# Kernel optimization log

Measured on AMD Instinct MI355X. Metric: run time of the kernel, lower is better.

## Reference

```python
import jax, jax.numpy as jnp
import numpy as np

M, D, A, H = 16384, 256, 264, 8
HD = A // H  # 33
B = 512
THRESH = 0.1
DECAY = 0.95


def setup_inputs() -> dict:
    key = jax.random.key(0)
    ks = jax.random.split(key, 16)
    rn = lambda i, shape, scale=1.0: jax.random.normal(ks[i], shape, dtype=jnp.float32) * scale
    return {
        "features": rn(0, (B, D)),
        "gradients": rn(1, (B, D), 0.1),
        "mem_keys": rn(2, (M, D)),
        "mem_values": rn(3, (M, D)),
        "mem_ages": jax.random.uniform(ks[4], (M,), dtype=jnp.float32, minval=0.0, maxval=50.0),
        "mem_surprise": jax.random.uniform(ks[5], (M,), dtype=jnp.float32, minval=0.0, maxval=5.0),
        "Wk": rn(6, (D, D), 1.0 / np.sqrt(D)), "bk": jnp.zeros((D,), jnp.float32),
        "Wv": rn(7, (D, D), 1.0 / np.sqrt(D)), "bv": jnp.zeros((D,), jnp.float32),
        "Wp": rn(8, (D, A), 1.0 / np.sqrt(D)), "bp": jnp.zeros((A,), jnp.float32),
        "Win": rn(9, (A, 3 * A), 1.0 / np.sqrt(A)), "b_in": jnp.zeros((3 * A,), jnp.float32),
        "Wout": rn(10, (A, A), 1.0 / np.sqrt(A)), "bout": jnp.zeros((A,), jnp.float32),
        "Wo": rn(11, (A, D), 1.0 / np.sqrt(A)), "bo": jnp.zeros((D,), jnp.float32),
    }


def reference(features, gradients, mem_keys, mem_values, mem_ages, mem_surprise,
              Wk, bk, Wv, bv, Wp, bp, Win, b_in, Wout, bout, Wo, bo):
    # ---- compute_surprise: grad norm * min cdist to memory keys ----
    d2 = (jnp.sum(features * features, 1)[:, None]
          + jnp.sum(mem_keys * mem_keys, 1)[None, :]
          - 2.0 * features @ mem_keys.T)                      # [B, M]
    min_dist = jnp.sqrt(jnp.clip(jnp.min(d2, axis=1), 0.0))   # [B]
    surprise = jnp.linalg.norm(gradients, axis=-1) * min_dist  # [B]
    memorize = surprise > THRESH                               # [B] bool

    # ---- write_memory: sequential per-item eviction (argmin of decayed surprise) ----
    def step(carry, xs):
        mk, mv, ages, surp = carry
        feat, s_i, w = xs
        slot = jnp.argmin(surp * DECAY ** ages)
        mk = mk.at[slot].set(jnp.where(w, feat @ Wk + bk, mk[slot]))
        mv = mv.at[slot].set(jnp.where(w, feat @ Wv + bv, mv[slot]))
        ages = ages.at[slot].set(jnp.where(w, 0.0, ages[slot]))
        surp = surp.at[slot].set(jnp.where(w, s_i, surp[slot]))
        return (mk, mv, ages, surp), None

    (mem_keys, mem_values, mem_ages, mem_surprise), _ = jax.lax.scan(
        step, (mem_keys, mem_values, mem_ages, mem_surprise),
        (features, surprise, memorize))

    # ---- read_memory: project, 8-head cross attention (1 query vs M slots) ----
    q = features @ Wp + bp        # [B, A]
    kf = mem_keys @ Wp + bp       # [M, A]
    vf = mem_values @ Wp + bp     # [M, A]
    Wq_, Wk_, Wv_ = jnp.split(Win, 3, axis=1)
    bq_, bk_, bv_ = jnp.split(b_in, 3)
    qh = (q @ Wq_ + bq_).reshape(B, H, HD)
    kh = (kf @ Wk_ + bk_).reshape(M, H, HD)
    vh = (vf @ Wv_ + bv_).reshape(M, H, HD)
    scores = jnp.einsum('bhd,mhd->bhm', qh, kh) / np.float32(np.sqrt(HD))
    attn = jax.nn.softmax(scores, axis=-1)                    # [B, H, M]
    ctx = jnp.einsum('bhm,mhd->bhd', attn, vh).reshape(B, A)
    retrieved = (ctx @ Wout + bout) @ Wo + bo                 # [B, D]
    return retrieved
```

## Files before the change

kernel.cpp:

```cpp
#include <hip/hip_runtime.h>
#include <math.h>
#include <stdint.h>

typedef unsigned short ushort_t;
typedef float v4f __attribute__((ext_vector_type(4)));
typedef short v8s __attribute__((ext_vector_type(8)));

#define ATTN_MS 16

__device__ __forceinline__ unsigned fenc(float f){
  unsigned b = __float_as_uint(f);
  return (b & 0x80000000u) ? ~b : (b | 0x80000000u);
}
__device__ __forceinline__ float fdec(unsigned u){
  unsigned b = (u & 0x80000000u) ? (u ^ 0x80000000u) : ~u;
  return __uint_as_float(b);
}
__device__ __forceinline__ ushort_t bf16_rne(float x){
  unsigned u = __float_as_uint(x);
  unsigned r = u + 0x7FFFu + ((u >> 16) & 1u);
  return (ushort_t)(r >> 16);
}
__device__ __forceinline__ void split2(float x, ushort_t& h, ushort_t& l){
  unsigned u = __float_as_uint(x);
  unsigned r = u + 0x7FFFu + ((u >> 16) & 1u);
  h = (ushort_t)(r >> 16);
  float hf = __uint_as_float(r & 0xFFFF0000u);
  l = bf16_rne(x - hf);
}
__device__ __forceinline__ float bf2f(ushort_t x){ return __uint_as_float(((unsigned)x) << 16); }
union U8 { v8s v; ushort_t u[8]; };

__device__ __forceinline__ void gl2lds16(const void* g, void* l){
  __builtin_amdgcn_global_load_lds(
      (const __attribute__((address_space(1))) unsigned int*)(uintptr_t)g,
      (__attribute__((address_space(3))) unsigned int*)(unsigned int)(uintptr_t)l,
      16, 0, 0);
}

__global__ __launch_bounds__(256) void prep_all(
    const float* __restrict__ features, const float* __restrict__ gradients,
    const float* __restrict__ mem_keys, const float* __restrict__ mem_values,
    ushort_t* __restrict__ FH, ushort_t* __restrict__ FL,
    ushort_t* __restrict__ MKH, ushort_t* __restrict__ MKL,
    ushort_t* __restrict__ MVH, ushort_t* __restrict__ MVL,
    float* __restrict__ k2, float* __restrict__ f2, float* __restrict__ gn,
    unsigned* __restrict__ minD2, ushort_t* __restrict__ VtGH, ushort_t* __restrict__ VtGL){
  int y = blockIdx.y, bx = blockIdx.x, t = threadIdx.x;
  if (y == 3){
    if (bx >= 3840) return;
    const int PER4 = 8*15*16384/4;
    int idx = bx*256 + t;
    if (idx >= 2*PER4) return;
    ushort_t* base = (idx < PER4) ? VtGH : VtGL;
    int i = (idx < PER4) ? idx : idx - PER4;
    int s = i*4;
    int hh = s / (15*16384);
    int r2 = s - hh*(15*16384);
    int row = 33 + (r2 >> 14);
    int col = r2 & 16383;
    ushort4 z; z.x = 0; z.y = 0; z.z = 0; z.w = 0;
    *(ushort4*)(base + (size_t)(hh*48 + row)*16384 + col) = z;
    return;
  }
  int wid = t >> 6, lane = t & 63;
  int row = bx*4 + wid;
  if (y == 2 && bx >= 128) return;
  const float* src = (y == 0) ? mem_keys : (y == 1) ? mem_values : features;
  float4 v = *(const float4*)(src + (size_t)row*256 + lane*4);
  ushort_t h0,h1,h2,h3,l0,l1,l2,l3;
  split2(v.x,h0,l0); split2(v.y,h1,l1); split2(v.z,h2,l2); split2(v.w,h3,l3);
  uint2 hp = make_uint2((unsigned)h0 | ((unsigned)h1<<16), (unsigned)h2 | ((unsigned)h3<<16));
  uint2 lp = make_uint2((unsigned)l0 | ((unsigned)l1<<16), (unsigned)l2 | ((unsigned)l3<<16));
  ushort_t* H = (y == 0) ? MKH : (y == 1) ? MVH : FH;
  ushort_t* L = (y == 0) ? MKL : (y == 1) ? MVL : FL;
  *(uint2*)(H + (size_t)row*256 + lane*4) = hp;
  *(uint2*)(L + (size_t)row*256 + lane*4) = lp;
  if (y == 1) return;
  float s = v.x*v.x + v.y*v.y + v.z*v.z + v.w*v.w;
  if (y == 0){
    for (int off = 32; off > 0; off >>= 1) s += __shfl_down(s, off, 64);
    if (lane == 0) k2[row] = s;
  } else {
    float4 g = *(const float4*)(gradients + (size_t)row*256 + lane*4);
    float tg = g.x*g.x + g.y*g.y + g.z*g.z + g.w*g.w;
    for (int off = 32; off > 0; off >>= 1){ s += __shfl_down(s, off, 64); tg += __shfl_down(tg, off, 64); }
    if (lane == 0){ f2[row] = s; gn[row] = sqrtf(tg); minD2[row] = 0xFFFFFFFFu; }
  }
}

__global__ __launch_bounds__(256) void gemm_bias(const float* __restrict__ A, const float* __restrict__ W,
                                                 const float* __restrict__ bias, float* __restrict__ C,
                                                 const float* __restrict__ W2, const float* __restrict__ bias2,
                                                 float* __restrict__ C2,
                                                 int M, int K, int N, int ldw, int woff){
  if (blockIdx.z == 1){ W = W2; bias = bias2; C = C2; }
  __shared__ float As[32*68];
  __shared__ float Ws[32*68];
  int m0 = blockIdx.x*64, c0 = blockIdx.y*64;
  int t = threadIdx.x;
  int mq = (t & 15)*4, cq = (t >> 4)*4;
  float acc[16];
  #pragma unroll
  for (int i = 0; i < 16; ++i) acc[i] = 0.f;
  for (int k0 = 0; k0 < K; k0 += 32){
    #pragma unroll
    for (int i = 0; i < 2; ++i){
      int idx = t + 256*i;
      int row = idx >> 3, kk = (idx & 7)*4;
      int gm = m0 + row, gk = k0 + kk;
      float x=0.f, y=0.f, z=0.f, w=0.f;
      if (gm < M){
        const float* ap = A + (size_t)gm*K + gk;
        if (gk + 3 < K){ float4 v = *(const float4*)ap; x=v.x; y=v.y; z=v.z; w=v.w; }
        else {
          if (gk   < K) x = ap[0];
          if (gk+1 < K) y = ap[1];
          if (gk+2 < K) z = ap[2];
          if (gk+3 < K) w = ap[3];
        }
      }
      As[(kk+0)*68+row]=x; As[(kk+1)*68+row]=y; As[(kk+2)*68+row]=z; As[(kk+3)*68+row]=w;
    }
    #pragma unroll
    for (int i = 0; i < 2; ++i){
      int idx = t + 256*i;
      int kk = idx >> 4, cc = (idx & 15)*4;
      int gk = k0 + kk, gc = c0 + cc;
      float4 v = make_float4(0.f,0.f,0.f,0.f);
      if (gk < K){
        const float* wp = W + (size_t)gk*ldw + woff + gc;
        if (gc + 3 < N) v = *(const float4*)wp;
        else {
          if (gc   < N) v.x = wp[0];
          if (gc+1 < N) v.y = wp[1];
          if (gc+2 < N) v.z = wp[2];
          if (gc+3 < N) v.w = wp[3];
        }
      }
      *(float4*)(Ws + kk*68 + cc) = v;
    }
    __syncthreads();
    #pragma unroll
    for (int j = 0; j < 32; ++j){
      float4 a = *(const float4*)(As + j*68 + mq);
      float4 w = *(const float4*)(Ws + j*68 + cq);
      acc[ 0]+=a.x*w.x; acc[ 1]+=a.x*w.y; acc[ 2]+=a.x*w.z; acc[ 3]+=a.x*w.w;
      acc[ 4]+=a.y*w.x; acc[ 5]+=a.y*w.y; acc[ 6]+=a.y*w.z; acc[ 7]+=a.y*w.w;
      acc[ 8]+=a.z*w.x; acc[ 9]+=a.z*w.y; acc[10]+=a.z*w.z; acc[11]+=a.z*w.w;
      acc[12]+=a.w*w.x; acc[13]+=a.w*w.y; acc[14]+=a.w*w.z; acc[15]+=a.w*w.w;
    }
    __syncthreads();
  }
  #pragma unroll
  for (int i = 0; i < 4; ++i){
    int gm = m0 + mq + i;
    if (gm >= M) continue;
    #pragma unroll
    for (int j = 0; j < 4; ++j){
      int gc = c0 + cq + j;
      if (gc >= N) continue;
      C[(size_t)gm*N + gc] = acc[i*4+j] + (bias ? bias[gc] : 0.f);
    }
  }
}

__global__ __launch_bounds__(256) void wprep_gemm(
    const float* __restrict__ Wp, const float* __restrict__ Win,
    const float* __restrict__ Wout, const float* __restrict__ Wo,
    const float* __restrict__ bp, const float* __restrict__ b_in,
    const float* __restrict__ bout, const float* __restrict__ bo,
    ushort_t* __restrict__ WtkH, ushort_t* __restrict__ WtkL,
    ushort_t* __restrict__ WtvH, ushort_t* __restrict__ WtvL,
    ushort_t* __restrict__ WtqH, ushort_t* __restrict__ WtqL,
    float* __restrict__ Wpk, float* __restrict__ Wpv, float* __restrict__ Wco,
    float* __restrict__ bpq, float* __restrict__ bpk, float* __restrict__ bpv, float* __restrict__ bco){
  __shared__ float As[32*68];
  __shared__ float Ws[32*68];
  int z = blockIdx.z;
  int t = threadIdx.x;
  if (z == 4){
    int flat = (blockIdx.x*5 + blockIdx.y)*256 + t;
    if (flat < 264){
      float a = b_in[flat];
      for (int k = 0; k < 264; ++k) a += bp[k]*Win[(size_t)k*792 + flat];
      bpq[flat] = a;
    } else if (flat < 528){
      int c = flat - 264;
      float a = b_in[264 + c];
      for (int k = 0; k < 264; ++k) a += bp[k]*Win[(size_t)k*792 + 264 + c];
      bpk[c] = a;
    } else if (flat < 792){
      int c = flat - 528;
      float a = b_in[528 + c];
      for (int k = 0; k < 264; ++k) a += bp[k]*Win[(size_t)k*792 + 528 + c];
      bpv[c] = a;
    } else if (flat < 1048){
      int c = flat - 792;
      float a = bo[c];
      for (int k = 0; k < 264; ++k) a += bout[k]*Wo[(size_t)k*256 + c];
      bco[c] = a;
    }
    return;
  }
  const float* A = (z < 3) ? Wp : Wout;
  const float* W = (z < 3) ? Win : Wo;
  const int M = (z < 3) ? 256 : 264;
  const int K = 264;
  const int N = (z < 3) ? 264 : 256;
  const int ldw = (z < 3) ? 792 : 256;
  const int woff = (z == 0) ? 264 : (z == 1) ? 528 : 0;
  int m0 = blockIdx.x*64, c0 = blockIdx.y*64;
  int mq = (t & 15)*4, cq = (t >> 4)*4;
  float acc[16];
  #pragma unroll
  for (int i = 0; i < 16; ++i) acc[i] = 0.f;
  for (int k0 = 0; k0 < K; k0 += 32){
    #pragma unroll
    for (int i = 0; i < 2; ++i){
      int idx = t + 256*i;
      int row = idx >> 3, kk = (idx & 7)*4;
      int gm = m0 + row, gk = k0 + kk;
      float x=0.f, y=0.f, z2=0.f, w=0.f;
      if (gm < M){
        const float* ap = A + (size_t)gm*K + gk;
        if (gk + 3 < K){ float4 v = *(const float4*)ap; x=v.x; y=v.y; z2=v.z; w=v.w; }
        else {
          if (gk   < K) x = ap[0];
          if (gk+1 < K) y = ap[1];
          if (gk+2 < K) z2 = ap[2];
          if (gk+3 < K) w = ap[3];
        }
      }
      As[(kk+0)*68+row]=x; As[(kk+1)*68+row]=y; As[(kk+2)*68+row]=z2; As[(kk+3)*68+row]=w;
    }
    #pragma unroll
    for (int i = 0; i < 2; ++i){
      int idx = t + 256*i;
      int kk = idx >> 4, cc = (idx & 15)*4;
      int gk = k0 + kk, gc = c0 + cc;
      float4 v = make_float4(0.f,0.f,0.f,0.f);
      if (gk < K){
        const float* wp = W + (size_t)gk*ldw + woff + gc;
        if (gc + 3 < N) v = *(const float4*)wp;
        else {
          if (gc   < N) v.x = wp[0];
          if (gc+1 < N) v.y = wp[1];
          if (gc+2 < N) v.z = wp[2];
          if (gc+3 < N) v.w = wp[3];
        }
      }
      *(float4*)(Ws + kk*68 + cc) = v;
    }
    __syncthreads();
    #pragma unroll
    for (int j = 0; j < 32; ++j){
      float4 a = *(const float4*)(As + j*68 + mq);
      float4 w = *(const float4*)(Ws + j*68 + cq);
      acc[ 0]+=a.x*w.x; acc[ 1]+=a.x*w.y; acc[ 2]+=a.x*w.z; acc[ 3]+=a.x*w.w;
      acc[ 4]+=a.y*w.x; acc[ 5]+=a.y*w.y; acc[ 6]+=a.y*w.z; acc[ 7]+=a.y*w.w;
      acc[ 8]+=a.z*w.x; acc[ 9]+=a.z*w.y; acc[10]+=a.z*w.z; acc[11]+=a.z*w.w;
      acc[12]+=a.w*w.x; acc[13]+=a.w*w.y; acc[14]+=a.w*w.z; acc[15]+=a.w*w.w;
    }
    __syncthreads();
  }
  if (z < 3){
    ushort_t* WH = (z==0) ? WtkH : (z==1) ? WtvH : WtqH;
    ushort_t* WL = (z==0) ? WtkL : (z==1) ? WtvL : WtqL;
    float* Wf = (z==0) ? Wpk : (z==1) ? Wpv : nullptr;
    #pragma unroll
    for (int i = 0; i < 4; ++i){
      int gm = m0 + mq + i;
      if (gm >= 256) continue;
      #pragma unroll
      for (int j = 0; j < 4; ++j){
        int gc = c0 + cq + j;
        float r = acc[i*4+j];
        ushort_t hh, ll; split2(r, hh, ll);
        WH[(size_t)gc*256 + gm] = hh;
        WL[(size_t)gc*256 + gm] = ll;
        if (Wf && gc < 264) Wf[(size_t)gm*264 + gc] = r;
      }
    }
  } else {
    #pragma unroll
    for (int i = 0; i < 4; ++i){
      int gm = m0 + mq + i;
      if (gm >= 264) continue;
      #pragma unroll
      for (int j = 0; j < 4; ++j){
        int gc = c0 + cq + j;
        if (gc < 256) Wco[(size_t)gm*256 + gc] = acc[i*4+j];
      }
    }
  }
}

__global__ __launch_bounds__(256, 4) void big_mfma(
    const ushort_t* __restrict__ FH, const ushort_t* __restrict__ FL,
    const ushort_t* __restrict__ MKH, const ushort_t* __restrict__ MKL,
    const ushort_t* __restrict__ MVH, const ushort_t* __restrict__ MVL,
    const ushort_t* __restrict__ WtqH, const ushort_t* __restrict__ WtqL,
    const ushort_t* __restrict__ WtkH, const ushort_t* __restrict__ WtkL,
    const ushort_t* __restrict__ WtvH, const ushort_t* __restrict__ WtvL,
    const float* __restrict__ bpq, const float* __restrict__ bpk, const float* __restrict__ bpv,
    const float* __restrict__ k2,
    float* __restrict__ qh, ushort_t* __restrict__ khH, ushort_t* __restrict__ khL,
    ushort_t* __restrict__ VtGH, ushort_t* __restrict__ VtGL, unsigned* __restrict__ minD2){
  int z = blockIdx.z;
  int bx = blockIdx.x, by = blockIdx.y;
  if (z == 0 && bx >= 4) return;
  if (z != 3 && by >= 5) return;
  __shared__ ushort_t AsH[128*32];
  __shared__ ushort_t AsL[128*32];
  __shared__ ushort_t BsH[64*32];
  __shared__ ushort_t BsL[64*32];
  __shared__ unsigned sminU[64];
  const ushort_t* AH = (z == 0) ? FH : (z == 2) ? MVH : MKH;
  const ushort_t* AL = (z == 0) ? FL : (z == 2) ? MVL : MKL;
  const ushort_t* BH = (z == 0) ? WtqH : (z == 1) ? WtkH : (z == 2) ? WtvH : FH;
  const ushort_t* BL = (z == 0) ? WtqL : (z == 1) ? WtkL : WtvL;
  const float* bias = (z == 0) ? bpq : (z == 1) ? bpk : bpv;
  int t = threadIdx.x;
  int m0 = bx*128, n0 = by*64;
  int lane = t & 63, w = t >> 6;
  int wm = (w & 1)*64, wn = (w >> 1)*32;
  int l15 = lane & 15, q = lane >> 4;
  if (z == 3 && t < 64) sminU[t] = 0xFFFFFFFFu;
  v4f acc[4][2];
  #pragma unroll
  for (int i = 0; i < 4; ++i)
    #pragma unroll
    for (int j = 0; j < 2; ++j) acc[i][j] = (v4f){0.f,0.f,0.f,0.f};

  for (int k0 = 0; k0 < 256; k0 += 32){
    #pragma unroll
    for (int c = 0; c < 2; ++c){
      int u0 = (c*4 + w)*64;
      int u  = u0 + lane;
      int row = u >> 2, ch = u & 3;
      gl2lds16(AH + (size_t)(m0+row)*256 + k0 + ch*8, AsH + (size_t)u0*8);
      if (z < 3) gl2lds16(AL + (size_t)(m0+row)*256 + k0 + ch*8, AsL + (size_t)u0*8);
    }
    {
      int u = w*64 + lane;
      int row = u >> 2, ch = u & 3;
      gl2lds16(BH + (size_t)(n0+row)*256 + k0 + ch*8, BsH + (size_t)w*512);
      if (z < 3) gl2lds16(BL + (size_t)(n0+row)*256 + k0 + ch*8, BsL + (size_t)w*512);
    }
    __syncthreads();
    if (z < 3){
      v8s aH[4], aL[4], bH[2], bL[2];
      #pragma unroll
      for (int im = 0; im < 4; ++im){
        aH[im] = *(const v8s*)(AsH + (wm + im*16 + l15)*32 + q*8);
        aL[im] = *(const v8s*)(AsL + (wm + im*16 + l15)*32 + q*8);
      }
      #pragma unroll
      for (int jn = 0; jn < 2; ++jn){
        bH[jn] = *(const v8s*)(BsH + (wn + jn*16 + l15)*32 + q*8);
        bL[jn] = *(const v8s*)(BsL + (wn + jn*16 + l15)*32 + q*8);
      }
      #pragma unroll
      for (int im = 0; im < 4; ++im)
        #pragma unroll
        for (int jn = 0; jn < 2; ++jn){
          acc[im][jn] = __builtin_amdgcn_mfma_f32_16x16x32_bf16(aH[im], bH[jn], acc[im][jn], 0, 0, 0);
          acc[im][jn] = __builtin_amdgcn_mfma_f32_16x16x32_bf16(aH[im], bL[jn], acc[im][jn], 0, 0, 0);
          acc[im][jn] = __builtin_amdgcn_mfma_f32_16x16x32_bf16(aL[im], bH[jn], acc[im][jn], 0, 0, 0);
        }
    } else {
      v8s aH[4], bH[2];
      #pragma unroll
      for (int im = 0; im < 4; ++im) aH[im] = *(const v8s*)(AsH + (wm + im*16 + l15)*32 + q*8);
      #pragma unroll
      for (int jn = 0; jn < 2; ++jn) bH[jn] = *(const v8s*)(BsH + (wn + jn*16 + l15)*32 + q*8);
      #pragma unroll
      for (int im = 0; im < 4; ++im)
        #pragma unroll
        for (int jn = 0; jn < 2; ++jn)
          acc[im][jn] = __builtin_amdgcn_mfma_f32_16x16x32_bf16(aH[im], bH[jn], acc[im][jn], 0, 0, 0);
    }
    __syncthreads();
  }

  if (z == 3){
    float kk[4][4];
    #pragma unroll
    for (int im = 0; im < 4; ++im)
      #pragma unroll
      for (int r = 0; r < 4; ++r) kk[im][r] = k2[m0 + wm + im*16 + q*4 + r];
    #pragma unroll
    for (int jn = 0; jn < 2; ++jn){
      float mv = INFINITY;
      #pragma unroll
      for (int im = 0; im < 4; ++im)
        #pragma unroll
        for (int r = 0; r < 4; ++r)
          mv = fminf(mv, kk[im][r] - 2.f*acc[im][jn][r]);
      mv = fminf(mv, __shfl_xor(mv, 16, 64));
      mv = fminf(mv, __shfl_xor(mv, 32, 64));
      if (q == 0) atomicMin(&sminU[wn + jn*16 + l15], fenc(mv));
    }
    __syncthreads();
    if (t < 64) atomicMin(&minD2[n0 + t], sminU[t]);
    return;
  }
  #pragma unroll
  for (int im = 0; im < 4; ++im){
    #pragma unroll
    for (int jn = 0; jn < 2; ++jn){
      int n = n0 + wn + jn*16 + l15;
      if (n >= 264) continue;
      float bv = bias[n];
      int mb = m0 + wm + im*16 + q*4;
      if (z == 0){
        #pragma unroll
        for (int r = 0; r < 4; ++r) qh[(size_t)(mb+r)*264 + n] = acc[im][jn][r] + bv;
      } else if (z == 1){
        int hh = n/33, dd = n - hh*33;
        int col = hh*40 + dd;
        #pragma unroll
        for (int r = 0; r < 4; ++r){
          ushort_t sh, sl; split2(acc[im][jn][r] + bv, sh, sl);
          khH[(size_t)(mb+r)*320 + col] = sh;
          khL[(size_t)(mb+r)*320 + col] = sl;
        }
      } else {
        int hh = n/33, dd = n - hh*33;
        size_t rowb = (size_t)(hh*48 + dd)*16384 + mb;
        ushort4 hv, lv;
        split2(acc[im][jn][0] + bv, hv.x, lv.x);
        split2(acc[im][jn][1] + bv, hv.y, lv.y);
        split2(acc[im][jn][2] + bv, hv.z, lv.z);
        split2(acc[im][jn][3] + bv, hv.w, lv.w);
        *(ushort4*)(VtGH + rowb) = hv;
        *(ushort4*)(VtGL + rowb) = lv;
      }
    }
  }
}

#define SCAN_CAP 1024
__global__ __launch_bounds__(1024) void scan_kernel(
    const float* __restrict__ mem_surprise, const float* __restrict__ mem_ages,
    const unsigned* __restrict__ minD2, const float* __restrict__ f2, const float* __restrict__ gn,
    float* __restrict__ parr, int* __restrict__ slotForB, int* __restrict__ lastB){
  __shared__ unsigned hist[2048];
  __shared__ float candV[SCAN_CAP];
  __shared__ int   candI[SCAN_CAP];
  __shared__ float tv[1024];
  __shared__ int   ti[1024];
  __shared__ float ssur[512];
  __shared__ int   smemz[512];
  __shared__ int   wtot[16];
  __shared__ int   sh_misc[8];
  int t = threadIdx.x;

  int mem = 0;
  if (t < 512){
    float d2 = fdec(minD2[t]) + f2[t];
    float s = gn[t]*sqrtf(fmaxf(d2, 0.f));
    ssur[t] = s;
    mem = (s > 0.1f) ? 1 : 0;
    smemz[t] = mem;
  }
  const float LN095 = -0.05129329438755058f;
  #pragma unroll
  for (int j = 0; j < 16; ++j){
    int m = t*16 + j;
    float p = mem_surprise[m] * __expf(mem_ages[m] * LN095);
    parr[m] = p;
    lastB[m] = -1;
  }
  hist[t] = 0u; hist[t + 1024] = 0u;
  if (t < 8) sh_misc[t] = (t == 3) ? 0x7F800000 : 0;
  __syncthreads();
  #pragma unroll
  for (int j = 0; j < 16; ++j){
    int m = t*16 + j;
    unsigned key = __float_as_uint(parr[m]) >> 20;
    if (key > 2047u) key = 2047u;
    atomicAdd(&hist[key], 1u);
  }
  __syncthreads();
  if (t < 512){ ti[t] = (int)(hist[4*t] + hist[4*t+1] + hist[4*t+2] + hist[4*t+3]); }
  __syncthreads();
  if (t < 32){ int s = 0; for (int i = 0; i < 16; ++i) s += ti[16*t + i]; ti[512 + t] = s; }
  __syncthreads();
  if (t == 0){
    int cum = 0, i2 = 0;
    for (; i2 < 32; ++i2){ if (cum + ti[512+i2] >= 512) break; cum += ti[512+i2]; }
    int i1 = i2*16;
    for (;; ++i1){ if (cum + ti[i1] >= 512) break; cum += ti[i1]; }
    int bin = i1*4;
    for (;; ++bin){ if (cum + (int)hist[bin] >= 512) break; cum += (int)hist[bin]; }
    sh_misc[1] = bin;
  }
  __syncthreads();
  int threshKey = sh_misc[1];
  #pragma unroll
  for (int j = 0; j < 16; ++j){
    int m = t*16 + j;
    unsigned key = __float_as_uint(parr[m]) >> 20;
    if (key > 2047u) key = 2047u;
    if ((int)key <= threshKey){
      int pos = atomicAdd(&sh_misc[0], 1);
      if (pos < SCAN_CAP){ candV[pos] = parr[m]; candI[pos] = m; }
    }
  }
  __syncthreads();
  int cnt = sh_misc[0];
  if (t >= cnt && t < SCAN_CAP){ candV[t] = INFINITY; candI[t] = 0x7FFFFFFF; }
  __syncthreads();
  for (int ksz = 2; ksz <= SCAN_CAP; ksz <<= 1){
    for (int jj = ksz >> 1; jj > 0; jj >>= 1){
      int ixj = t ^ jj;
      if (ixj > t){
        float v1 = candV[t], v2 = candV[ixj];
        int i1 = candI[t], i2 = candI[ixj];
        bool lt21 = (v2 < v1) || (v2 == v1 && i2 < i1);
        bool lt12 = (v1 < v2) || (v1 == v2 && i1 < i2);
        bool up = ((t & ksz) == 0);
        bool sw = up ? lt21 : lt12;
        if (sw){ candV[t] = v2; candI[t] = i2; candV[ixj] = v1; candI[ixj] = i1; }
      }
      __syncthreads();
    }
  }
  int lp = 0;
  if (t < 512){
    unsigned long long mask = __ballot(mem != 0);
    int lane = t & 63;
    lp = __popcll(mask & ((1ull << lane) - 1ull));
    if (lane == 0) wtot[t >> 6] = __popcll(mask);
  }
  if (t < 512 && mem) atomicMin(&sh_misc[3], __float_as_int(ssur[t]));
  __syncthreads();
  if (t == 0){
    int ksum = 0;
    for (int wv = 0; wv < 8; ++wv) ksum += wtot[wv];
    sh_misc[4] = ksum;
    bool okf = (cnt <= SCAN_CAP) && (ksum <= cnt);
    if (okf && ksum > 0){
      float minw = __int_as_float(sh_misc[3]);
      okf = (minw > candV[ksum - 1]);
    }
    sh_misc[2] = okf ? 1 : 0;
  }
  __syncthreads();
  if (sh_misc[2] == 1){
    if (t < 512){
      int wv = t >> 6, base = 0;
      for (int i = 0; i < wv; ++i) base += wtot[i];
      int slot = -1;
      if (mem){ slot = candI[base + lp]; atomicMax(&lastB[slot], t); }
      slotForB[t] = slot;
    }
  } else {
    for (int b = 0; b < 512; ++b){
      float bv = parr[t*16]; int bi = t*16;
      #pragma unroll
      for (int j = 1; j < 16; ++j){
        float v = parr[t*16 + j];
        if (v < bv){ bv = v; bi = t*16 + j; }
      }
      tv[t] = bv; ti[t] = bi;
      __syncthreads();
      for (int s = 512; s > 0; s >>= 1){
        if (t < s){
          float v2 = tv[t+s]; int i2 = ti[t+s];
          if (v2 < tv[t] || (v2 == tv[t] && i2 < ti[t])){ tv[t] = v2; ti[t] = i2; }
        }
        __syncthreads();
      }
      int slot = ti[0];
      int memb = smemz[b];
      if (t == 0) slotForB[b] = memb ? slot : -1;
      if (memb && t == (slot >> 4)) parr[slot] = ssur[b];
      __syncthreads();
    }
    if (t < 512){ int s = slotForB[t]; if (s >= 0) atomicMax(&lastB[s], t); }
  }
}

__global__ __launch_bounds__(64) void fixup_rows(const int* __restrict__ slotForB, const int* __restrict__ lastB,
                                                 const float* __restrict__ newK, const float* __restrict__ newV,
                                                 const float* __restrict__ Wpk, const float* __restrict__ Wpv,
                                                 const float* __restrict__ bpk, const float* __restrict__ bpv,
                                                 ushort_t* __restrict__ khH, ushort_t* __restrict__ khL,
                                                 ushort_t* __restrict__ VtH, ushort_t* __restrict__ VtL){
  int b = blockIdx.x;
  int slot = slotForB[b];
  if (slot < 0) return;
  if (lastB[slot] != b) return;
  __shared__ float kr[256], vr[256];
  int t = threadIdx.x;
  *(float4*)(kr + t*4) = *(const float4*)(newK + (size_t)b*256 + t*4);
  *(float4*)(vr + t*4) = *(const float4*)(newV + (size_t)b*256 + t*4);
  __syncthreads();
  for (int c = t; c < 264; c += 64){
    float aK = bpk[c], aV = bpv[c];
    for (int k = 0; k < 256; ++k){
      aK += kr[k]*Wpk[(size_t)k*264 + c];
      aV += vr[k]*Wpv[(size_t)k*264 + c];
    }
    int hh = c/33, dd = c - hh*33;
    ushort_t sh, sl;
    split2(aK, sh, sl);
    khH[(size_t)slot*320 + hh*40 + dd] = sh;
    khL[(size_t)slot*320 + hh*40 + dd] = sl;
    split2(aV, sh, sl);
    VtH[(size_t)(hh*48 + dd)*16384 + slot] = sh;
    VtL[(size_t)(hh*48 + dd)*16384 + slot] = sl;
  }
}

__global__ __launch_bounds__(256, 4) void attn_mfma(
    const float* __restrict__ qh, const ushort_t* __restrict__ khH, const ushort_t* __restrict__ khL,
    const ushort_t* __restrict__ VtGH, const ushort_t* __restrict__ VtGL,
    float* __restrict__ pm, float* __restrict__ pl, float* __restrict__ pctx){
  const int h = blockIdx.x, bt = blockIdx.y, ms = blockIdx.z;
  const int b0 = bt*64, mbase = ms*(16384/ATTN_MS);
  const int t = threadIdx.x, lane = t & 63, w = t >> 6;
  const int l15 = lane & 15, q = lane >> 4;
  __shared__ ushort_t KH[64*32], KL[64*32];
  __shared__ ushort_t VsH[48*64], VsL[48*64];
  __shared__ ushort_t PH[4*16*72], PL[4*16*72];
  __shared__ float k32f[64];
  const float scale = 0.17407765595569785f;

  const int bq = b0 + 16*w + l15;
  U8 qHU, qLU;
  {
    const float* qp = qh + (size_t)bq*264 + h*33 + q*8;
    #pragma unroll
    for (int j = 0; j < 8; ++j) split2(qp[j]*scale, qHU.u[j], qLU.u[j]);
  }
  const v8s bQH = qHU.v, bQL = qLU.v;
  const float q32v = qh[(size_t)bq*264 + h*33 + 32]*scale;
  float rMv = -INFINITY, rLv = 0.f;
  v4f cacc[3];
  #pragma unroll
  for (int i = 0; i < 3; ++i) cacc[i] = (v4f){0.f,0.f,0.f,0.f};
  ushort_t* PHw = PH + w*16*72;
  ushort_t* PLw = PL + w*16*72;

  for (int mt = 0; mt < 16384/ATTN_MS/64; ++mt){
    const int m0 = mbase + mt*64;
    __syncthreads();
    {
      int u = w*64 + lane;
      int row = u >> 2, ch = u & 3;
      gl2lds16(khH + (size_t)(m0+row)*320 + h*40 + ch*8, KH + (size_t)w*512);
      gl2lds16(khL + (size_t)(m0+row)*320 + h*40 + ch*8, KL + (size_t)w*512);
    }
    if (t < 64)
      k32f[t] = bf2f(khH[(size_t)(m0+t)*320 + h*40 + 32]) + bf2f(khL[(size_t)(m0+t)*320 + h*40 + 32]);
    #pragma unroll
    for (int c = 0; c < 2; ++c){
      if (c == 0 || w < 2){
        int u0 = c*256 + w*64;
        int u = u0 + lane;
        int dd = u >> 3, chl = u & 7;
        int gch = chl ^ (dd & 7);
        size_t gi = (size_t)(h*48 + dd)*16384 + m0 + gch*8;
        gl2lds16(VtGH + gi, VsH + (size_t)u0*8);
        gl2lds16(VtGL + gi, VsL + (size_t)u0*8);
      }
    }
    __syncthreads();
    v4f s4[4];
    #pragma unroll
    for (int im = 0; im < 4; ++im){
      v8s aH = *(const v8s*)(KH + (im*16 + l15)*32 + q*8);
      v8s aL = *(const v8s*)(KL + (im*16 + l15)*32 + q*8);
      v4f sv = (v4f){0.f,0.f,0.f,0.f};
      sv = __builtin_amdgcn_mfma_f32_16x16x32_bf16(aH, bQH, sv, 0, 0, 0);
      sv = __builtin_amdgcn_mfma_f32_16x16x32_bf16(aH, bQL, sv, 0, 0, 0);
      sv = __builtin_amdgcn_mfma_f32_16x16x32_bf16(aL, bQH, sv, 0, 0, 0);
      s4[im] = sv;
    }
    #pragma unroll
    for (int im = 0; im < 4; ++im)
      #pragma unroll
      for (int r = 0; r < 4; ++r) s4[im][r] += k32f[im*16 + q*4 + r]*q32v;
    float mx = -INFINITY;
    #pragma unroll
    for (int im = 0; im < 4; ++im)
      #pragma unroll
      for (int r = 0; r < 4; ++r) mx = fmaxf(mx, s4[im][r]);
    mx = fmaxf(mx, __shfl_xor(mx, 16, 64));
    mx = fmaxf(mx, __shfl_xor(mx, 32, 64));
    float nm = fmaxf(rMv, mx);
    float alf = __expf(rMv - nm);
    rMv = nm;
    float sm = 0.f;
    #pragma unroll
    for (int im = 0; im < 4; ++im){
      v4f p;
      #pragma unroll
      for (int r = 0; r < 4; ++r){ p[r] = __expf(s4[im][r] - nm); sm += p[r]; }
      ushort4 hv, lv;
      split2(p[0], hv.x, lv.x); split2(p[1], hv.y, lv.y);
      split2(p[2], hv.z, lv.z); split2(p[3], hv.w, lv.w);
      *(ushort4*)(PHw + l15*72 + im*16 + q*4) = hv;
      *(ushort4*)(PLw + l15*72 + im*16 + q*4) = lv;
    }
    sm += __shfl_xor(sm, 16, 64);
    sm += __shfl_xor(sm, 32, 64);
    rLv = rLv*alf + sm;
    #pragma unroll
    for (int r = 0; r < 4; ++r){
      float ar = __shfl(alf, q*4 + r, 64);
      cacc[0][r] *= ar; cacc[1][r] *= ar; cacc[2][r] *= ar;
    }
    #pragma unroll
    for (int ks = 0; ks < 2; ++ks){
      v8s paH = *(const v8s*)(PHw + l15*72 + ks*32 + q*8);
      v8s paL = *(const v8s*)(PLw + l15*72 + ks*32 + q*8);
      #pragma unroll
      for (int tile = 0; tile < 3; ++tile){
        int vrow = tile*16 + l15;
        int mch = (ks*4 + q) ^ (l15 & 7);
        v8s vbH = *(const v8s*)(VsH + vrow*64 + mch*8);
        v8s vbL = *(const v8s*)(VsL + vrow*64 + mch*8);
        cacc[tile] = __builtin_amdgcn_mfma_f32_16x16x32_bf16(paH, vbH, cacc[tile], 0, 0, 0);
        cacc[tile] = __builtin_amdgcn_mfma_f32_16x16x32_bf16(paH, vbL, cacc[tile], 0, 0, 0);
        cacc[tile] = __builtin_amdgcn_mfma_f32_16x16x32_bf16(paL, vbH, cacc[tile], 0, 0, 0);
      }
    }
  }
  int g = (h*8 + bt)*ATTN_MS + ms;
  if (q == 0){
    pm[(size_t)g*64 + 16*w + l15] = rMv;
    pl[(size_t)g*64 + 16*w + l15] = rLv;
  }
  #pragma unroll
  for (int tile = 0; tile < 3; ++tile){
    int d = tile*16 + l15;
    if (d < 33){
      #pragma unroll
      for (int r = 0; r < 4; ++r)
        pctx[((size_t)g*64 + 16*w + q*4 + r)*33 + d] = cacc[tile][r];
    }
  }
}

__global__ __launch_bounds__(256) void combine_kernel(const float* __restrict__ pm, const float* __restrict__ pl,
                                                      const float* __restrict__ pctx, float* __restrict__ ctxf){
  int idx = blockIdx.x*256 + threadIdx.x;
  if (idx >= 512*264) return;
  int b = idx / 264, c = idx - b*264;
  int h = c / 33, d = c - h*33;
  int bt = b >> 6, bl = b & 63;
  int g0 = (h*8 + bt)*ATTN_MS;
  float gm = -INFINITY;
  for (int ms = 0; ms < ATTN_MS; ++ms) gm = fmaxf(gm, pm[(g0+ms)*64 + bl]);
  float L = 0.f, cv = 0.f;
  for (int ms = 0; ms < ATTN_MS; ++ms){
    int gg = (g0+ms)*64 + bl;
    float w = __expf(pm[gg] - gm);
    L += pl[gg]*w;
    cv += pctx[(size_t)gg*33 + d]*w;
  }
  ctxf[idx] = cv / L;
}

extern "C" void kernel_launch(void* const* d_in, const int* in_sizes, int n_in,
                              void* d_out, int out_size, void* d_ws, size_t ws_size,
                              hipStream_t stream){
  (void)in_sizes; (void)n_in; (void)out_size; (void)ws_size;
  const float* features     = (const float*)d_in[0];
  const float* gradients    = (const float*)d_in[1];
  const float* mem_keys     = (const float*)d_in[2];
  const float* mem_values   = (const float*)d_in[3];
  const float* mem_ages     = (const float*)d_in[4];
  const float* mem_surprise = (const float*)d_in[5];
  const float* Wk   = (const float*)d_in[6];
  const float* bk   = (const float*)d_in[7];
  const float* Wv   = (const float*)d_in[8];
  const float* bv   = (const float*)d_in[9];
  const float* Wp   = (const float*)d_in[10];
  const float* bp   = (const float*)d_in[11];
  const float* Win  = (const float*)d_in[12];
  const float* b_in = (const float*)d_in[13];
  const float* Wout = (const float*)d_in[14];
  const float* bout = (const float*)d_in[15];
  const float* Wo   = (const float*)d_in[16];
  const float* bo   = (const float*)d_in[17];
  float* out = (float*)d_out;

  float* w = (float*)d_ws;
  size_t off = 0;
  auto alloc = [&](size_t n)->float*{ float* p = w + off; off += (n + 63) & ~(size_t)63; return p; };
  float*    k2       = alloc(16384);
  unsigned* minD2    = (unsigned*)alloc(512);
  float*    f2       = alloc(512);
  float*    gn       = alloc(512);
  int*      slotForB = (int*)alloc(512);
  int*      lastB    = (int*)alloc(16384);
  float*    parr     = alloc(16384);
  float*    newK     = alloc((size_t)512*256);
  float*    newV     = alloc((size_t)512*256);
  float*    qh       = alloc((size_t)512*264);
  ushort_t* khH      = (ushort_t*)alloc((size_t)16384*320/2);
  ushort_t* khL      = (ushort_t*)alloc((size_t)16384*320/2);
  ushort_t* VtGH     = (ushort_t*)alloc((size_t)8*48*16384/2);
  ushort_t* VtGL     = (ushort_t*)alloc((size_t)8*48*16384/2);
  float*    MKbase   = alloc((size_t)16384*256/2*2);
  ushort_t* MKH      = (ushort_t*)MKbase;
  ushort_t* MKL      = (ushort_t*)(MKbase + (size_t)16384*256/2);
  float*    MVbase   = alloc((size_t)16384*256/2*2);
  ushort_t* MVH      = (ushort_t*)MVbase;
  ushort_t* MVL      = (ushort_t*)(MVbase + (size_t)16384*256/2);
  ushort_t* FH       = (ushort_t*)alloc((size_t)512*256/2);
  ushort_t* FL       = (ushort_t*)alloc((size_t)512*256/2);
  float*    Wpk      = alloc((size_t)256*264);
  float*    Wpv      = alloc((size_t)256*264);
  float*    Wco      = alloc((size_t)264*256);
  ushort_t* WtkH     = (ushort_t*)alloc((size_t)320*256/2);
  ushort_t* WtkL     = (ushort_t*)alloc((size_t)320*256/2);
  ushort_t* WtvH     = (ushort_t*)alloc((size_t)320*256/2);
  ushort_t* WtvL     = (ushort_t*)alloc((size_t)320*256/2);
  ushort_t* WtqH     = (ushort_t*)alloc((size_t)320*256/2);
  ushort_t* WtqL     = (ushort_t*)alloc((size_t)320*256/2);
  float*    bpq      = alloc(264);
  float*    bpk      = alloc(264);
  float*    bpv      = alloc(264);
  float*    bco      = alloc(256);
  float*    pm       = MKbase;
  float*    pl       = MKbase + (size_t)ATTN_MS*64*64;
  float*    ctxf     = pl + (size_t)ATTN_MS*64*64;
  float*    pctx     = MVbase;

  prep_all<<<dim3(4096,4), 256, 0, stream>>>(features, gradients, mem_keys, mem_values,
      FH, FL, MKH, MKL, MVH, MVL, k2, f2, gn, minD2, VtGH, VtGL);

  wprep_gemm<<<dim3(5,5,5), 256, 0, stream>>>(Wp, Win, Wout, Wo, bp, b_in, bout, bo,
      WtkH, WtkL, WtvH, WtvL, WtqH, WtqL, Wpk, Wpv, Wco, bpq, bpk, bpv, bco);

  gemm_bias<<<dim3(8,4,2), 256, 0, stream>>>(features, Wk, bk, newK, Wv, bv, newV, 512, 256, 256, 256, 0);

  big_mfma<<<dim3(128,8,4), 256, 0, stream>>>(FH, FL, MKH, MKL, MVH, MVL,
      WtqH, WtqL, WtkH, WtkL, WtvH, WtvL, bpq, bpk, bpv, k2,
      qh, khH, khL, VtGH, VtGL, minD2);

  scan_kernel<<<1, 1024, 0, stream>>>(mem_surprise, mem_ages, minD2, f2, gn, parr, slotForB, lastB);
  fixup_rows<<<512, 64, 0, stream>>>(slotForB, lastB, newK, newV, Wpk, Wpv, bpk, bpv, khH, khL, VtGH, VtGL);

  attn_mfma<<<dim3(8,8,ATTN_MS), 256, 0, stream>>>(qh, khH, khL, VtGH, VtGL, pm, pl, pctx);
  combine_kernel<<<528, 256, 0, stream>>>(pm, pl, pctx, ctxf);
  gemm_bias<<<dim3(8,4,1), 256, 0, stream>>>(ctxf, Wco, bco, out, Wco, bco, out, 512, 264, 256, 256, 0);
}
```

Measured before the change: 398.8 us.

## Fold Wk/Wv into projection weights, precompute replacement rows, drop V padding zeroing

Precomputes the combined weights Wk·Wpk and Wv·Wpv (plus biases) in a new wprep2 kernel. big_mfma then gets two extra z-slices that compute the projected replacement key and value rows for all 512 features with MFMA. fixup_rows becomes a plain copy instead of a serial 256-long dot product per column. It also removes the big zero-fill of VtG padding rows in prep_all, zeroing those rows once in LDS inside attn_mfma instead. The k32 scalar column is stored as fp32 in a separate buffer and loaded asynchronously, where before it was reconstructed from bf16 halves. The extra work is a few small launches and blocks, and replacement rows are now rounded through a folded weight product, which changes the rounding order slightly.

```diff
diff --git a/kernel.cpp b/kernel.cpp
--- a/kernel.cpp
+++ b/kernel.cpp
@@ -28,7 +28,6 @@
   float hf = __uint_as_float(r & 0xFFFF0000u);
   l = bf16_rne(x - hf);
 }
-__device__ __forceinline__ float bf2f(ushort_t x){ return __uint_as_float(((unsigned)x) << 16); }
 union U8 { v8s v; ushort_t u[8]; };
 
 __device__ __forceinline__ void gl2lds16(const void* g, void* l){
@@ -45,24 +44,8 @@
     ushort_t* __restrict__ MKH, ushort_t* __restrict__ MKL,
     ushort_t* __restrict__ MVH, ushort_t* __restrict__ MVL,
     float* __restrict__ k2, float* __restrict__ f2, float* __restrict__ gn,
-    unsigned* __restrict__ minD2, ushort_t* __restrict__ VtGH, ushort_t* __restrict__ VtGL){
+    unsigned* __restrict__ minD2){
   int y = blockIdx.y, bx = blockIdx.x, t = threadIdx.x;
-  if (y == 3){
-    if (bx >= 3840) return;
-    const int PER4 = 8*15*16384/4;
-    int idx = bx*256 + t;
-    if (idx >= 2*PER4) return;
-    ushort_t* base = (idx < PER4) ? VtGH : VtGL;
-    int i = (idx < PER4) ? idx : idx - PER4;
-    int s = i*4;
-    int hh = s / (15*16384);
-    int r2 = s - hh*(15*16384);
-    int row = 33 + (r2 >> 14);
-    int col = r2 & 16383;
-    ushort4 z; z.x = 0; z.y = 0; z.z = 0; z.w = 0;
-    *(ushort4*)(base + (size_t)(hh*48 + row)*16384 + col) = z;
-    return;
-  }
   int wid = t >> 6, lane = t & 63;
   int row = bx*4 + wid;
   if (y == 2 && bx >= 128) return;
@@ -91,10 +74,7 @@
 
 __global__ __launch_bounds__(256) void gemm_bias(const float* __restrict__ A, const float* __restrict__ W,
                                                  const float* __restrict__ bias, float* __restrict__ C,
-                                                 const float* __restrict__ W2, const float* __restrict__ bias2,
-                                                 float* __restrict__ C2,
                                                  int M, int K, int N, int ldw, int woff){
-  if (blockIdx.z == 1){ W = W2; bias = bias2; C = C2; }
   __shared__ float As[32*68];
   __shared__ float Ws[32*68];
   int m0 = blockIdx.x*64, c0 = blockIdx.y*64;
@@ -296,6 +276,91 @@
   }
 }
 
+__global__ __launch_bounds__(256) void wprep2(
+    const float* __restrict__ Wk, const float* __restrict__ Wv,
+    const float* __restrict__ Wpk, const float* __restrict__ Wpv,
+    const float* __restrict__ bk, const float* __restrict__ bv,
+    const float* __restrict__ bpk, const float* __restrict__ bpv,
+    ushort_t* __restrict__ WtfkH, ushort_t* __restrict__ WtfkL,
+    ushort_t* __restrict__ WtfvH, ushort_t* __restrict__ WtfvL,
+    float* __restrict__ bfk, float* __restrict__ bfv){
+  __shared__ float As[32*68];
+  __shared__ float Ws[32*68];
+  int z = blockIdx.z;
+  int t = threadIdx.x;
+  if (z == 2){
+    int flat = (blockIdx.x*5 + blockIdx.y)*256 + t;
+    if (flat < 264){
+      float a = bpk[flat];
+      for (int k = 0; k < 256; ++k) a += bk[k]*Wpk[(size_t)k*264 + flat];
+      bfk[flat] = a;
+    } else if (flat < 528){
+      int c = flat - 264;
+      float a = bpv[c];
+      for (int k = 0; k < 256; ++k) a += bv[k]*Wpv[(size_t)k*264 + c];
+      bfv[c] = a;
+    }
+    return;
+  }
+  if (blockIdx.x >= 4) return;
+  const float* A = z ? Wv : Wk;
+  const float* W = z ? Wpv : Wpk;
+  int m0 = blockIdx.x*64, c0 = blockIdx.y*64;
+  int mq = (t & 15)*4, cq = (t >> 4)*4;
+  float acc[16];
+  #pragma unroll
+  for (int i = 0; i < 16; ++i) acc[i] = 0.f;
+  for (int k0 = 0; k0 < 256; k0 += 32){
+    #pragma unroll
+    for (int i = 0; i < 2; ++i){
+      int idx = t + 256*i;
+      int row = idx >> 3, kk = (idx & 7)*4;
+      float4 v = *(const float4*)(A + (size_t)(m0+row)*256 + k0 + kk);
+      As[(kk+0)*68+row]=v.x; As[(kk+1)*68+row]=v.y; As[(kk+2)*68+row]=v.z; As[(kk+3)*68+row]=v.w;
+    }
+    #pragma unroll
+    for (int i = 0; i < 2; ++i){
+      int idx = t + 256*i;
+      int kk = idx >> 4, cc = (idx & 15)*4;
+      int gk = k0 + kk, gc = c0 + cc;
+      float4 v = make_float4(0.f,0.f,0.f,0.f);
+      const float* wp = W + (size_t)gk*264 + gc;
+      if (gc + 3 < 264) v = *(const float4*)wp;
+      else {
+        if (gc   < 264) v.x = wp[0];
+        if (gc+1 < 264) v.y = wp[1];
+        if (gc+2 < 264) v.z = wp[2];
+        if (gc+3 < 264) v.w = wp[3];
+      }
+      *(float4*)(Ws + kk*68 + cc) = v;
+    }
+    __syncthreads();
+    #pragma unroll
+    for (int j = 0; j < 32; ++j){
+      float4 a = *(const float4*)(As + j*68 + mq);
+      float4 w = *(const float4*)(Ws + j*68 + cq);
+      acc[ 0]+=a.x*w.x; acc[ 1]+=a.x*w.y; acc[ 2]+=a.x*w.z; acc[ 3]+=a.x*w.w;
+      acc[ 4]+=a.y*w.x; acc[ 5]+=a.y*w.y; acc[ 6]+=a.y*w.z; acc[ 7]+=a.y*w.w;
+      acc[ 8]+=a.z*w.x; acc[ 9]+=a.z*w.y; acc[10]+=a.z*w.z; acc[11]+=a.z*w.w;
+      acc[12]+=a.w*w.x; acc[13]+=a.w*w.y; acc[14]+=a.w*w.z; acc[15]+=a.w*w.w;
+    }
+    __syncthreads();
+  }
+  ushort_t* WH = z ? WtfvH : WtfkH;
+  ushort_t* WL = z ? WtfvL : WtfkL;
+  #pragma unroll
+  for (int i = 0; i < 4; ++i){
+    int gm = m0 + mq + i;
+    #pragma unroll
+    for (int j = 0; j < 4; ++j){
+      int gc = c0 + cq + j;
+      ushort_t hh, ll; split2(acc[i*4+j], hh, ll);
+      WH[(size_t)gc*256 + gm] = hh;
+      WL[(size_t)gc*256 + gm] = ll;
+    }
+  }
+}
+
 __global__ __launch_bounds__(256, 4) void big_mfma(
     const ushort_t* __restrict__ FH, const ushort_t* __restrict__ FL,
     const ushort_t* __restrict__ MKH, const ushort_t* __restrict__ MKL,
@@ -303,24 +368,29 @@
     const ushort_t* __restrict__ WtqH, const ushort_t* __restrict__ WtqL,
     const ushort_t* __restrict__ WtkH, const ushort_t* __restrict__ WtkL,
     const ushort_t* __restrict__ WtvH, const ushort_t* __restrict__ WtvL,
+    const ushort_t* __restrict__ WtfkH, const ushort_t* __restrict__ WtfkL,
+    const ushort_t* __restrict__ WtfvH, const ushort_t* __restrict__ WtfvL,
     const float* __restrict__ bpq, const float* __restrict__ bpk, const float* __restrict__ bpv,
+    const float* __restrict__ bfk, const float* __restrict__ bfv,
     const float* __restrict__ k2,
-    float* __restrict__ qh, ushort_t* __restrict__ khH, ushort_t* __restrict__ khL,
+    float* __restrict__ qh, float* __restrict__ khB, float* __restrict__ VtB,
+    ushort_t* __restrict__ khH, ushort_t* __restrict__ khL, float* __restrict__ k32g,
     ushort_t* __restrict__ VtGH, ushort_t* __restrict__ VtGL, unsigned* __restrict__ minD2){
   int z = blockIdx.z;
   int bx = blockIdx.x, by = blockIdx.y;
-  if (z == 0 && bx >= 4) return;
+  if ((z == 0 || z >= 4) && bx >= 4) return;
   if (z != 3 && by >= 5) return;
   __shared__ ushort_t AsH[128*32];
   __shared__ ushort_t AsL[128*32];
   __shared__ ushort_t BsH[64*32];
   __shared__ ushort_t BsL[64*32];
   __shared__ unsigned sminU[64];
-  const ushort_t* AH = (z == 0) ? FH : (z == 2) ? MVH : MKH;
-  const ushort_t* AL = (z == 0) ? FL : (z == 2) ? MVL : MKL;
-  const ushort_t* BH = (z == 0) ? WtqH : (z == 1) ? WtkH : (z == 2) ? WtvH : FH;
-  const ushort_t* BL = (z == 0) ? WtqL : (z == 1) ? WtkL : WtvL;
-  const float* bias = (z == 0) ? bpq : (z == 1) ? bpk : bpv;
+  const ushort_t* AH = (z == 2) ? MVH : (z == 1 || z == 3) ? MKH : FH;
+  const ushort_t* AL = (z == 2) ? MVL : (z == 1 || z == 3) ? MKL : FL;
+  const ushort_t* BH = (z==0) ? WtqH : (z==1) ? WtkH : (z==2) ? WtvH : (z==3) ? FH : (z==4) ? WtfkH : WtfvH;
+  const ushort_t* BL = (z==0) ? WtqL : (z==1) ? WtkL : (z==2) ? WtvL : (z==4) ? WtfkL : WtfvL;
+  const float* bias = (z==0) ? bpq : (z==1) ? bpk : (z==2) ? bpv : (z==4) ? bfk : bfv;
+  float* Cf = (z==0) ? qh : (z==4) ? khB : VtB;
   int t = threadIdx.x;
   int m0 = bx*128, n0 = by*64;
   int lane = t & 63, w = t >> 6;
@@ -340,16 +410,16 @@
       int u  = u0 + lane;
       int row = u >> 2, ch = u & 3;
       gl2lds16(AH + (size_t)(m0+row)*256 + k0 + ch*8, AsH + (size_t)u0*8);
-      if (z < 3) gl2lds16(AL + (size_t)(m0+row)*256 + k0 + ch*8, AsL + (size_t)u0*8);
+      if (z != 3) gl2lds16(AL + (size_t)(m0+row)*256 + k0 + ch*8, AsL + (size_t)u0*8);
     }
     {
       int u = w*64 + lane;
       int row = u >> 2, ch = u & 3;
       gl2lds16(BH + (size_t)(n0+row)*256 + k0 + ch*8, BsH + (size_t)w*512);
-      if (z < 3) gl2lds16(BL + (size_t)(n0+row)*256 + k0 + ch*8, BsL + (size_t)w*512);
-    }
-    __syncthreads();
-    if (z < 3){
+      if (z != 3) gl2lds16(BL + (size_t)(n0+row)*256 + k0 + ch*8, BsL + (size_t)w*512);
+    }
+    __syncthreads();
+    if (z != 3){
       v8s aH[4], aL[4], bH[2], bL[2];
       #pragma unroll
       for (int im = 0; im < 4; ++im){
@@ -414,19 +484,18 @@
       if (n >= 264) continue;
       float bv = bias[n];
       int mb = m0 + wm + im*16 + q*4;
-      if (z == 0){
-        #pragma unroll
-        for (int r = 0; r < 4; ++r) qh[(size_t)(mb+r)*264 + n] = acc[im][jn][r] + bv;
-      } else if (z == 1){
+      if (z == 1){
         int hh = n/33, dd = n - hh*33;
         int col = hh*40 + dd;
         #pragma unroll
         for (int r = 0; r < 4; ++r){
-          ushort_t sh, sl; split2(acc[im][jn][r] + bv, sh, sl);
+          float val = acc[im][jn][r] + bv;
+          ushort_t sh, sl; split2(val, sh, sl);
           khH[(size_t)(mb+r)*320 + col] = sh;
           khL[(size_t)(mb+r)*320 + col] = sl;
+          if (dd == 32) k32g[(size_t)hh*16384 + mb + r] = val;
         }
-      } else {
+      } else if (z == 2){
         int hh = n/33, dd = n - hh*33;
         size_t rowb = (size_t)(hh*48 + dd)*16384 + mb;
         ushort4 hv, lv;
@@ -436,6 +505,9 @@
         split2(acc[im][jn][3] + bv, hv.w, lv.w);
         *(ushort4*)(VtGH + rowb) = hv;
         *(ushort4*)(VtGL + rowb) = lv;
+      } else {
+        #pragma unroll
+        for (int r = 0; r < 4; ++r) Cf[(size_t)(mb+r)*264 + n] = acc[im][jn][r] + bv;
       }
     }
   }
@@ -585,32 +657,25 @@
 }
 
 __global__ __launch_bounds__(64) void fixup_rows(const int* __restrict__ slotForB, const int* __restrict__ lastB,
-                                                 const float* __restrict__ newK, const float* __restrict__ newV,
-                                                 const float* __restrict__ Wpk, const float* __restrict__ Wpv,
-                                                 const float* __restrict__ bpk, const float* __restrict__ bpv,
+                                                 const float* __restrict__ khB, const float* __restrict__ VtB,
                                                  ushort_t* __restrict__ khH, ushort_t* __restrict__ khL,
-                                                 ushort_t* __restrict__ VtH, ushort_t* __restrict__ VtL){
+                                                 ushort_t* __restrict__ VtH, ushort_t* __restrict__ VtL,
+                                                 float* __restrict__ k32g){
   int b = blockIdx.x;
   int slot = slotForB[b];
   if (slot < 0) return;
   if (lastB[slot] != b) return;
-  __shared__ float kr[256], vr[256];
   int t = threadIdx.x;
-  *(float4*)(kr + t*4) = *(const float4*)(newK + (size_t)b*256 + t*4);
-  *(float4*)(vr + t*4) = *(const float4*)(newV + (size_t)b*256 + t*4);
-  __syncthreads();
   for (int c = t; c < 264; c += 64){
-    float aK = bpk[c], aV = bpv[c];
-    for (int k = 0; k < 256; ++k){
-      aK += kr[k]*Wpk[(size_t)k*264 + c];
-      aV += vr[k]*Wpv[(size_t)k*264 + c];
-    }
     int hh = c/33, dd = c - hh*33;
+    float kv = khB[(size_t)b*264 + c];
     ushort_t sh, sl;
-    split2(aK, sh, sl);
+    split2(kv, sh, sl);
     khH[(size_t)slot*320 + hh*40 + dd] = sh;
     khL[(size_t)slot*320 + hh*40 + dd] = sl;
-    split2(aV, sh, sl);
+    if (dd == 32) k32g[(size_t)hh*16384 + slot] = kv;
+    float vv = VtB[(size_t)b*264 + c];
+    split2(vv, sh, sl);
     VtH[(size_t)(hh*48 + dd)*16384 + slot] = sh;
     VtL[(size_t)(hh*48 + dd)*16384 + slot] = sl;
   }
@@ -618,7 +683,7 @@
 
 __global__ __launch_bounds__(256, 4) void attn_mfma(
     const float* __restrict__ qh, const ushort_t* __restrict__ khH, const ushort_t* __restrict__ khL,
-    const ushort_t* __restrict__ VtGH, const ushort_t* __restrict__ VtGL,
+    const ushort_t* __restrict__ VtGH, const ushort_t* __restrict__ VtGL, const float* __restrict__ k32g,
     float* __restrict__ pm, float* __restrict__ pl, float* __restrict__ pctx){
   const int h = blockIdx.x, bt = blockIdx.y, ms = blockIdx.z;
   const int b0 = bt*64, mbase = ms*(16384/ATTN_MS);
@@ -627,7 +692,7 @@
   __shared__ ushort_t KH[64*32], KL[64*32];
   __shared__ ushort_t VsH[48*64], VsL[48*64];
   __shared__ ushort_t PH[4*16*72], PL[4*16*72];
-  __shared__ float k32f[64];
+  __shared__ float k32fs[64];
   const float scale = 0.17407765595569785f;
 
   const int bq = b0 + 16*w + l15;
@@ -645,6 +710,12 @@
   for (int i = 0; i < 3; ++i) cacc[i] = (v4f){0.f,0.f,0.f,0.f};
   ushort_t* PHw = PH + w*16*72;
   ushort_t* PLw = PL + w*16*72;
+
+  {
+    unsigned* vh32 = (unsigned*)(VsH + 33*64);
+    unsigned* vl32 = (unsigned*)(VsL + 33*64);
+    for (int e = t; e < 480; e += 256){ vh32[e] = 0u; vl32[e] = 0u; }
+  }
 
   for (int mt = 0; mt < 16384/ATTN_MS/64; ++mt){
     const int m0 = mbase + mt*64;
@@ -654,19 +725,18 @@
       int row = u >> 2, ch = u & 3;
       gl2lds16(khH + (size_t)(m0+row)*320 + h*40 + ch*8, KH + (size_t)w*512);
       gl2lds16(khL + (size_t)(m0+row)*320 + h*40 + ch*8, KL + (size_t)w*512);
-    }
-    if (t < 64)
-      k32f[t] = bf2f(khH[(size_t)(m0+t)*320 + h*40 + 32]) + bf2f(khL[(size_t)(m0+t)*320 + h*40 + 32]);
-    #pragma unroll
-    for (int c = 0; c < 2; ++c){
-      if (c == 0 || w < 2){
-        int u0 = c*256 + w*64;
-        int u = u0 + lane;
-        int dd = u >> 3, chl = u & 7;
-        int gch = chl ^ (dd & 7);
-        size_t gi = (size_t)(h*48 + dd)*16384 + m0 + gch*8;
-        gl2lds16(VtGH + gi, VsH + (size_t)u0*8);
-        gl2lds16(VtGL + gi, VsL + (size_t)u0*8);
+      int dd = u >> 3, chl = u & 7;
+      int gch = chl ^ (dd & 7);
+      gl2lds16(VtGH + (size_t)(h*48 + dd)*16384 + m0 + gch*8, VsH + (size_t)w*512);
+      gl2lds16(VtGL + (size_t)(h*48 + dd)*16384 + m0 + gch*8, VsL + (size_t)w*512);
+    }
+    if (w == 0){
+      if (lane < 8){
+        gl2lds16(VtGH + (size_t)(h*48 + 32)*16384 + m0 + lane*8, VsH + 32*64);
+        gl2lds16(VtGL + (size_t)(h*48 + 32)*16384 + m0 + lane*8, VsL + 32*64);
+      }
+      if (lane < 16){
+        gl2lds16(k32g + ((size_t)h << 14) + m0 + lane*4, k32fs);
       }
     }
     __syncthreads();
@@ -682,9 +752,11 @@
       s4[im] = sv;
     }
     #pragma unroll
-    for (int im = 0; im < 4; ++im)
-      #pragma unroll
-      for (int r = 0; r < 4; ++r) s4[im][r] += k32f[im*16 + q*4 + r]*q32v;
+    for (int im = 0; im < 4; ++im){
+      float4 kv = *(const float4*)(k32fs + im*16 + q*4);
+      s4[im][0] += kv.x*q32v; s4[im][1] += kv.y*q32v;
+      s4[im][2] += kv.z*q32v; s4[im][3] += kv.w*q32v;
+    }
     float mx = -INFINITY;
     #pragma unroll
     for (int im = 0; im < 4; ++im)
@@ -801,9 +873,10 @@
   int*      slotForB = (int*)alloc(512);
   int*      lastB    = (int*)alloc(16384);
   float*    parr     = alloc(16384);
-  float*    newK     = alloc((size_t)512*256);
-  float*    newV     = alloc((size_t)512*256);
+  float*    khB      = alloc((size_t)512*264);
+  float*    VtB      = alloc((size_t)512*264);
   float*    qh       = alloc((size_t)512*264);
+  float*    k32g     = alloc((size_t)8*16384);
   ushort_t* khH      = (ushort_t*)alloc((size_t)16384*320/2);
   ushort_t* khL      = (ushort_t*)alloc((size_t)16384*320/2);
   ushort_t* VtGH     = (ushort_t*)alloc((size_t)8*48*16384/2);
@@ -825,31 +898,39 @@
   ushort_t* WtvL     = (ushort_t*)alloc((size_t)320*256/2);
   ushort_t* WtqH     = (ushort_t*)alloc((size_t)320*256/2);
   ushort_t* WtqL     = (ushort_t*)alloc((size_t)320*256/2);
+  ushort_t* WtfkH    = (ushort_t*)alloc((size_t)320*256/2);
+  ushort_t* WtfkL    = (ushort_t*)alloc((size_t)320*256/2);
+  ushort_t* WtfvH    = (ushort_t*)alloc((size_t)320*256/2);
+  ushort_t* WtfvL    = (ushort_t*)alloc((size_t)320*256/2);
   float*    bpq      = alloc(264);
   float*    bpk      = alloc(264);
   float*    bpv      = alloc(264);
   float*    bco      = alloc(256);
+  float*    bfk      = alloc(264);
+  float*    bfv      = alloc(264);
   float*    pm       = MKbase;
   float*    pl       = MKbase + (size_t)ATTN_MS*64*64;
   float*    ctxf     = pl + (size_t)ATTN_MS*64*64;
   float*    pctx     = MVbase;
 
-  prep_all<<<dim3(4096,4), 256, 0, stream>>>(features, gradients, mem_keys, mem_values,
-      FH, FL, MKH, MKL, MVH, MVL, k2, f2, gn, minD2, VtGH, VtGL);
+  prep_all<<<dim3(4096,3), 256, 0, stream>>>(features, gradients, mem_keys, mem_values,
+      FH, FL, MKH, MKL, MVH, MVL, k2, f2, gn, minD2);
 
   wprep_gemm<<<dim3(5,5,5), 256, 0, stream>>>(Wp, Win, Wout, Wo, bp, b_in, bout, bo,
       WtkH, WtkL, WtvH, WtvL, WtqH, WtqL, Wpk, Wpv, Wco, bpq, bpk, bpv, bco);
 
-  gemm_bias<<<dim3(8,4,2), 256, 0, stream>>>(features, Wk, bk, newK, Wv, bv, newV, 512, 256, 256, 256, 0);
-
-  big_mfma<<<dim3(128,8,4), 256, 0, stream>>>(FH, FL, MKH, MKL, MVH, MVL,
-      WtqH, WtqL, WtkH, WtkL, WtvH, WtvL, bpq, bpk, bpv, k2,
-      qh, khH, khL, VtGH, VtGL, minD2);
+  wprep2<<<dim3(5,5,3), 256, 0, stream>>>(Wk, Wv, Wpk, Wpv, bk, bv, bpk, bpv,
+      WtfkH, WtfkL, WtfvH, WtfvL, bfk, bfv);
+
+  big_mfma<<<dim3(128,8,6), 256, 0, stream>>>(FH, FL, MKH, MKL, MVH, MVL,
+      WtqH, WtqL, WtkH, WtkL, WtvH, WtvL, WtfkH, WtfkL, WtfvH, WtfvL,
+      bpq, bpk, bpv, bfk, bfv, k2,
+      qh, khB, VtB, khH, khL, k32g, VtGH, VtGL, minD2);
 
   scan_kernel<<<1, 1024, 0, stream>>>(mem_surprise, mem_ages, minD2, f2, gn, parr, slotForB, lastB);
-  fixup_rows<<<512, 64, 0, stream>>>(slotForB, lastB, newK, newV, Wpk, Wpv, bpk, bpv, khH, khL, VtGH, VtGL);
-
-  attn_mfma<<<dim3(8,8,ATTN_MS), 256, 0, stream>>>(qh, khH, khL, VtGH, VtGL, pm, pl, pctx);
+  fixup_rows<<<512, 64, 0, stream>>>(slotForB, lastB, khB, VtB, khH, khL, VtGH, VtGL, k32g);
+
+  attn_mfma<<<dim3(8,8,ATTN_MS), 256, 0, stream>>>(qh, khH, khL, VtGH, VtGL, k32g, pm, pl, pctx);
   combine_kernel<<<528, 256, 0, stream>>>(pm, pl, pctx, ctxf);
-  gemm_bias<<<dim3(8,4,1), 256, 0, stream>>>(ctxf, Wco, bco, out, Wco, bco, out, 512, 264, 256, 256, 0);
-}
+  gemm_bias<<<dim3(8,4), 256, 0, stream>>>(ctxf, Wco, bco, out, 512, 264, 256, 256, 0);
+}
```

New measurement: 346.2 us. 13.2% less time.
